# Kernel optimization log

Measured on AMD Instinct MI355X. Metric: run time of the kernel, lower is better.

Reference implementation:

```python
import jax, jax.numpy as jnp
import numpy as np

SELF_DIM = 64
OBST_DIM = 32
NUM_LANDMARKS = 8
HID = 128
IN_DIM = SELF_DIM + OBST_DIM  # 96


def setup_inputs() -> dict:
    key = jax.random.key(0)
    ks = jax.random.split(key, 16)
    B = 1024
    obs = jax.random.normal(ks[0], (B, 1, SELF_DIM + 40 + NUM_LANDMARKS * OBST_DIM), dtype=jnp.float32)

    def w(k, shape, fan_in):
        return (jax.random.normal(k, shape, dtype=jnp.float32) / np.sqrt(fan_in)).astype(jnp.float32)

    return {
        "obs": obs,
        "all_neighbor_obs_size": 40,
        "batch_size": B,
        # Hypernet2: Linear(96->128), tanh, Linear(128->96*128), tanh
        "hw1": w(ks[1], (IN_DIM, HID), IN_DIM), "hb1": jnp.zeros((HID,), jnp.float32),
        "hw2": w(ks[2], (HID, IN_DIM * HID), HID), "hb2": jnp.zeros((IN_DIM * HID,), jnp.float32),
        # neighbor_value_mlp: two Linear(128->128) with tanh
        "vw1": w(ks[3], (HID, HID), HID), "vb1": jnp.zeros((HID,), jnp.float32),
        "vw2": w(ks[4], (HID, HID), HID), "vb2": jnp.zeros((HID,), jnp.float32),
        # attention_mlp: Linear(256->128) tanh, Linear(128->128) tanh, Linear(128->1)
        "aw1": w(ks[5], (2 * HID, HID), 2 * HID), "ab1": jnp.zeros((HID,), jnp.float32),
        "aw2": w(ks[6], (HID, HID), HID), "ab2": jnp.zeros((HID,), jnp.float32),
        "aw3": w(ks[7], (HID, 1), HID), "ab3": jnp.zeros((1,), jnp.float32),
    }


def reference(obs, all_neighbor_obs_size, batch_size,
              hw1, hb1, hw2, hb2, vw1, vb1, vw2, vb2,
              aw1, ab1, aw2, ab2, aw3, ab3):
    B = batch_size
    A = obs.shape[1]  # agents per row (1)
    L = NUM_LANDMARKS

    # slice obstacle block and flatten to per-obstacle rows  [B*A*L, OBST_DIM]
    obs_obstacles = obs[:, :, SELF_DIM + all_neighbor_obs_size:].reshape(-1, OBST_DIM)
    # repeat self-obs along dim 1 (torch .repeat(1, L, 1)) -> [B*A*L, SELF_DIM]
    self_rep = jnp.tile(obs[:, :, :SELF_DIM], (1, L, 1)).reshape(-1, SELF_DIM)
    mlp_input = jnp.concatenate([self_rep, obs_obstacles], axis=1)  # [N, 96]
    N = mlp_input.shape[0]

    # Hypernet2 -> per-instance weight [N, 96, HID]
    h = jnp.tanh(mlp_input @ hw1 + hb1)
    w_flat = jnp.tanh(h @ hw2 + hb2)
    obstacle_w = w_flat.reshape(N, IN_DIM, HID)

    # per-instance matvec + tanh  [N, HID]
    emb = jnp.tanh(jnp.einsum('ni,nio->no', mlp_input, obstacle_w))

    # neighbor value MLP
    vals = jnp.tanh(jnp.tanh(emb @ vw1 + vb1) @ vw2 + vb2)

    # mean pooling over landmarks per batch
    emb_mean = emb.reshape(B, -1, HID).mean(axis=1)  # [B, HID]
    # torch mean.repeat(L, 1): tile whole batch block L times (faithful ordering)
    mean_rep = jnp.tile(emb_mean, (L, 1))  # [B*L, HID]

    att_in = jnp.concatenate([emb, mean_rep], axis=1)  # [N, 2*HID]
    a = jnp.tanh(att_in @ aw1 + ab1)
    a = jnp.tanh(a @ aw2 + ab2)
    logits = (a @ aw3 + ab3).reshape(B, -1)  # [B, L]
    att = jax.nn.softmax(logits, axis=1).reshape(-1, 1)  # [N, 1]

    final = (att * vals).reshape(B, -1, HID).sum(axis=1)  # [B, HID]
    return final.reshape(-1, A, HID)
```

## Files before the change

kernel.cpp:

```cpp
#include <hip/hip_runtime.h>

typedef _Float16 f16x8 __attribute__((ext_vector_type(8)));
typedef float f32x4 __attribute__((ext_vector_type(4)));
typedef const __attribute__((address_space(1))) void* as1_cvp;
typedef __attribute__((address_space(3))) void* as3_vp;

#define LOG2E2 2.88539008177793f

__device__ __forceinline__ float tanh_fast(float x){
  float e = __builtin_amdgcn_exp2f(x * LOG2E2);
  return 1.f - 2.f * __builtin_amdgcn_rcpf(1.f + e);
}
__device__ __forceinline__ unsigned short f2h(float f){
  return __builtin_bit_cast(unsigned short, (_Float16)f);
}
__device__ __forceinline__ float h2f(unsigned short u){
  return (float)__builtin_bit_cast(_Float16, u);
}
__device__ __forceinline__ f32x4 mfma16(f16x8 a, f16x8 b, f32x4 c){
  return __builtin_amdgcn_mfma_f32_16x16x32_f16(a, b, c, 0, 0, 0);
}
__device__ __forceinline__ f16x8 ldsA(const unsigned short* buf, int rb, int s, int lane){
  return *(const f16x8*)(buf + (rb*16 + (lane&15))*128 + s*32 + ((lane>>4)<<3));
}

__global__ __launch_bounds__(256) void prep_kernel(
    const float* __restrict__ obs, const float* __restrict__ hw1,
    const float* __restrict__ hb1, const float* __restrict__ hw2,
    const float* __restrict__ vw1, const float* __restrict__ vw2,
    const float* __restrict__ aw1, const float* __restrict__ aw2,
    unsigned short* __restrict__ wt2, unsigned short* __restrict__ vw1t,
    unsigned short* __restrict__ vw2t, unsigned short* __restrict__ aw1t,
    unsigned short* __restrict__ aw2t, unsigned short* __restrict__ h16,
    float* __restrict__ xT){
  int b = blockIdx.x, t = threadIdx.x;
  if (b < 768){
    __shared__ float xp[64][33];
    int i = b >> 3, chalf = (b&7) >> 2, kq = b & 3;
    int c0 = i*128 + chalf*64, r0 = kq*32;
    int tx = t & 63, j0 = t >> 6;
    #pragma unroll
    for (int j = j0; j < 32; j += 4)
      xp[tx][j] = hw2[(size_t)(r0+j)*12288 + c0 + tx];
    __syncthreads();
    int c = t & 63, kgl = t >> 6;
    unsigned short us[8];
    #pragma unroll
    for (int q=0;q<8;++q) us[q] = f2h(xp[c][kgl*8 + q]);
    size_t dst = (size_t)(i*2 + chalf)*8192 + (size_t)(kq*4 + kgl)*512 + c*8;
    *(uint4*)(wt2 + dst) = *(uint4*)us;
  } else if (b < 848){
    __shared__ float tile[32][33];
    const float* in; unsigned short* out; int R, bx, by;
    if (b < 784)      { int q=b-768; in=vw1; out=vw1t; R=128; bx=q&3; by=q>>2; }
    else if (b < 800) { int q=b-784; in=vw2; out=vw2t; R=128; bx=q&3; by=q>>2; }
    else if (b < 832) { int q=b-800; in=aw1; out=aw1t; R=256; bx=q&3; by=q>>2; }
    else              { int q=b-832; in=aw2; out=aw2t; R=128; bx=q&3; by=q>>2; }
    int c0=bx*32, r0=by*32, tx=t&31, ty=t>>5;
    #pragma unroll
    for (int j=ty; j<32; j+=8) tile[j][tx] = in[(size_t)(r0+j)*128 + c0 + tx];
    __syncthreads();
    #pragma unroll
    for (int j=ty; j<32; j+=8) out[(size_t)(c0+j)*R + r0 + tx] = f2h(tile[tx][j]);
  } else {
    __shared__ float w_s[96*128];
    __shared__ float x_s[32*97];
    __shared__ float b_s[128];
    int n0 = (b-848)*32;
    for (int idx=t; idx<96*128; idx+=256) w_s[idx] = hw1[idx];
    if (t < 128) b_s[t] = hb1[t];
    for (int idx=t; idx<32*96; idx+=256){
      int r = idx/96, i = idx - r*96;
      int n = n0 + r; int bb = n>>3, l = n&7;
      x_s[r*97+i] = (i<64) ? obs[bb*360 + i] : obs[bb*360 + 104 + (l<<5) + (i-64)];
    }
    __syncthreads();
    for (int e=t; e<96*32; e+=256){
      int i = e>>5, r = e&31;
      xT[(size_t)i*8192 + n0 + r] = x_s[r*97 + i];
    }
    for (int e=t; e<32*128; e+=256){
      int r = e>>7, o = e&127;
      float acc = b_s[o];
      const float* xr = &x_s[r*97];
      #pragma unroll 4
      for (int i=0;i<96;++i) acc = fmaf(xr[i], w_s[i*128+o], acc);
      h16[(size_t)(n0+r)*128 + o] = f2h(tanh_fast(acc));
    }
  }
}

__device__ __forceinline__ void stage_tile(const unsigned short* gsrc,
                                           unsigned short* lbuf, int t){
  const unsigned short* g = gsrc + t*8;
  unsigned short* l = lbuf + t*8;
  #pragma unroll
  for (int p=0;p<4;++p)
    __builtin_amdgcn_global_load_lds((as1_cvp)(g + p*2048), (as3_vp)(l + p*2048), 16, 0, 0);
}

__global__ __launch_bounds__(256) __attribute__((amdgpu_waves_per_eu(3,4)))
void k2_hyper(const float* __restrict__ xT, const unsigned short* __restrict__ h16,
              const unsigned short* __restrict__ wt2, const float* __restrict__ hb2,
              float* __restrict__ accg){
  __shared__ unsigned short bts[2][8192];
  __shared__ float x_s[12*128];
  __shared__ float bias_s[12*64];
  int t = threadIdx.x, lane = t & 63, rg = t >> 6;
  int bid = blockIdx.x;
  int rt = bid >> 4, chalf = (bid >> 3) & 1, iseg = bid & 7;
  int R0 = rt*128, C0 = chalf*64, ibase = iseg*12;
  int cl   = lane & 15;
  int g    = lane >> 4;
  int kof  = g << 3;
  int rloc = g << 2;

  for (int idx=t; idx<12*128; idx+=256){
    int il = idx>>7, r = idx&127;
    x_s[idx] = xT[(size_t)(ibase+il)*8192 + R0 + r];
  }
  for (int idx=t; idx<12*64; idx+=256){
    int il = idx>>6, c = idx&63;
    bias_s[idx] = hb2[(ibase+il)*128 + C0 + c];
  }

  f16x8 af[2][4];
  #pragma unroll
  for (int rb=0; rb<2; ++rb)
    #pragma unroll
    for (int s=0; s<4; ++s)
      af[rb][s] = *(const f16x8*)(h16 + (size_t)(R0 + rg*32 + rb*16 + cl)*128 + s*32 + kof);

  stage_tile(wt2 + (size_t)(ibase*2 + chalf)*8192, bts[0], t);

  float facc[2][4][4];
  #pragma unroll
  for (int rb=0;rb<2;++rb)
    #pragma unroll
    for (int ch=0;ch<4;++ch)
      #pragma unroll
      for (int reg=0;reg<4;++reg) facc[rb][ch][reg] = 0.f;

  const f32x4 zero4 = {0.f,0.f,0.f,0.f};

  for (int it=0; it<12; ++it){
    asm volatile("s_waitcnt vmcnt(0)" ::: "memory");
    __builtin_amdgcn_s_barrier();
    __builtin_amdgcn_sched_barrier(0);
    const unsigned short* lb = bts[it&1];
    if (it < 11) stage_tile(wt2 + (size_t)((ibase+it+1)*2 + chalf)*8192, bts[(it+1)&1], t);

    f32x4 xa = *(const f32x4*)(x_s + it*128 + rg*32 + rloc);
    f32x4 xb = *(const f32x4*)(x_s + it*128 + rg*32 + 16 + rloc);
    #pragma unroll
    for (int ch=0; ch<4; ++ch){
      int c64 = ch*16 + cl;
      const unsigned short* bp = lb + c64*8 + g*512;
      f16x8 b0 = *(const f16x8*)(bp);
      f16x8 b1 = *(const f16x8*)(bp + 2048);
      f16x8 b2 = *(const f16x8*)(bp + 4096);
      f16x8 b3 = *(const f16x8*)(bp + 6144);
      float bi2 = bias_s[it*64 + c64] * LOG2E2;
      f32x4 a0 = zero4, a1 = zero4;
      a0 = mfma16(af[0][0], b0, a0); a1 = mfma16(af[1][0], b0, a1);
      a0 = mfma16(af[0][1], b1, a0); a1 = mfma16(af[1][1], b1, a1);
      a0 = mfma16(af[0][2], b2, a0); a1 = mfma16(af[1][2], b2, a1);
      a0 = mfma16(af[0][3], b3, a0); a1 = mfma16(af[1][3], b3, a1);
      #pragma unroll
      for (int reg=0;reg<4;++reg){
        float e0 = __builtin_amdgcn_exp2f(fmaf(a0[reg], LOG2E2, bi2));
        float e1 = __builtin_amdgcn_exp2f(fmaf(a1[reg], LOG2E2, bi2));
        float t0 = 1.f - 2.f*__builtin_amdgcn_rcpf(1.f + e0);
        float t1 = 1.f - 2.f*__builtin_amdgcn_rcpf(1.f + e1);
        facc[0][ch][reg] = fmaf(xa[reg], t0, facc[0][ch][reg]);
        facc[1][ch][reg] = fmaf(xb[reg], t1, facc[1][ch][reg]);
      }
    }
  }

  #pragma unroll
  for (int rb=0; rb<2; ++rb)
    #pragma unroll
    for (int ch=0; ch<4; ++ch)
      #pragma unroll
      for (int reg=0; reg<4; ++reg)
        atomicAdd(&accg[(size_t)(R0 + rg*32 + rb*16 + rloc + reg)*128 + C0 + ch*16 + cl],
                  facc[rb][ch][reg]);
}

__global__ __launch_bounds__(256) void k3_mean(const float* __restrict__ accg,
    unsigned short* __restrict__ mean16){
  int t = threadIdx.x, B0 = blockIdx.x*4;
  for (int task=t; task<512; task+=256){
    int bl = task>>7, o = task&127;
    float m = 0.f;
    #pragma unroll
    for (int l=0;l<8;++l)
      m += tanh_fast(accg[(size_t)((B0 + bl)*8 + l)*128 + o]);
    mean16[(size_t)(B0 + bl)*128 + o] = f2h(m * 0.125f);
  }
}

template<int KS>
__device__ __forceinline__ void stage(const unsigned short* inA, const unsigned short* inB,
    const unsigned short* wt, const float* bias, unsigned short* outb, int w, int lane){
  #pragma unroll
  for (int obl=0; obl<2; ++obl){
    int col = ((w*2+obl)<<4) + (lane&15);
    f32x4 a0 = {0.f,0.f,0.f,0.f}, a1v = {0.f,0.f,0.f,0.f};
    #pragma unroll
    for (int s=0;s<KS;++s){
      f16x8 bfr = *(const f16x8*)(wt + (size_t)col*(KS*32) + s*32 + ((lane>>4)<<3));
      f16x8 aa0, aa1;
      if (KS==8 && s>=4){ aa0 = ldsA(inB,0,s-4,lane); aa1 = ldsA(inB,1,s-4,lane); }
      else              { aa0 = ldsA(inA,0,s,lane);   aa1 = ldsA(inA,1,s,lane);   }
      a0  = mfma16(aa0, bfr, a0);
      a1v = mfma16(aa1, bfr, a1v);
    }
    float bb = bias[col];
    #pragma unroll
    for (int reg=0;reg<4;++reg){
      int r0 = ((lane>>4)<<2) + reg;
      outb[r0*128 + col]      = f2h(tanh_fast(a0[reg] + bb));
      outb[(16+r0)*128 + col] = f2h(tanh_fast(a1v[reg] + bb));
    }
  }
}

__global__ __launch_bounds__(256) void k4_mlp(
    const float* __restrict__ accg, const unsigned short* __restrict__ mean16,
    const unsigned short* __restrict__ vw1t, const unsigned short* __restrict__ vw2t,
    const unsigned short* __restrict__ aw1t, const unsigned short* __restrict__ aw2t,
    const float* __restrict__ vb1, const float* __restrict__ vb2,
    const float* __restrict__ ab1, const float* __restrict__ ab2,
    const float* __restrict__ aw3, const float* __restrict__ ab3,
    float* __restrict__ outp){
  __shared__ unsigned short bufE[32*128];
  __shared__ unsigned short bufM[32*128];
  __shared__ unsigned short bufA[32*128];
  __shared__ float fin[4*128];
  __shared__ float lp[32*8];
  __shared__ float att_s[32];
  int t = threadIdx.x, lane = t&63, w = t>>6;
  int R0 = blockIdx.x*32;

  for (int idx=t; idx<4096; idx+=256)
    bufE[idx] = f2h(tanh_fast(accg[(size_t)R0*128 + idx]));
  for (int idx=t; idx<512; idx+=256){
    int r = idx>>4, c8 = (idx&15)<<3;
    int n = R0 + r;
    *(uint4*)(bufM + r*128 + c8) = *(const uint4*)(mean16 + (size_t)(n & 1023)*128 + c8);
  }
  for (int idx=t; idx<512; idx+=256) fin[idx] = 0.f;
  __syncthreads();

  stage<8>(bufE, bufM, aw1t, ab1, bufA, w, lane);
  __syncthreads();
  stage<4>(bufA, nullptr, aw2t, ab2, bufM, w, lane);
  __syncthreads();
  {
    int r = t>>3, seg = t&7;
    float p = 0.f;
    const unsigned short* row = bufM + r*128 + seg*16;
    const float* w3 = aw3 + seg*16;
    #pragma unroll
    for (int k=0;k<16;++k) p += h2f(row[k]) * w3[k];
    lp[r*8+seg] = p;
  }
  __syncthreads();
  if (t < 4){
    float lg[8]; float mx = -1e30f;
    for (int l=0;l<8;++l){
      float s = ab3[0];
      #pragma unroll
      for (int sg=0;sg<8;++sg) s += lp[(t*8+l)*8+sg];
      lg[l] = s; mx = fmaxf(mx, s);
    }
    float sum = 0.f;
    for (int l=0;l<8;++l){ lg[l] = __builtin_amdgcn_exp2f((lg[l]-mx)*1.44269504089f); sum += lg[l]; }
    float inv = __builtin_amdgcn_rcpf(sum);
    for (int l=0;l<8;++l) att_s[t*8+l] = lg[l]*inv;
  }
  __syncthreads();
  stage<4>(bufE, nullptr, vw1t, vb1, bufA, w, lane);
  __syncthreads();
  {
    #pragma unroll
    for (int obl=0; obl<2; ++obl){
      int col = ((w*2+obl)<<4) + (lane&15);
      f32x4 a0 = {0.f,0.f,0.f,0.f}, a1v = {0.f,0.f,0.f,0.f};
      #pragma unroll
      for (int s=0;s<4;++s){
        f16x8 bfr = *(const f16x8*)(vw2t + (size_t)col*128 + s*32 + ((lane>>4)<<3));
        a0  = mfma16(ldsA(bufA,0,s,lane), bfr, a0);
        a1v = mfma16(ldsA(bufA,1,s,lane), bfr, a1v);
      }
      float bb = vb2[col];
      #pragma unroll
      for (int reg=0;reg<4;++reg){
        int r0 = ((lane>>4)<<2) + reg;
        float v0 = tanh_fast(a0[reg]+bb);
        float v1 = tanh_fast(a1v[reg]+bb);
        atomicAdd(&fin[((r0)>>3)*128 + col],    att_s[r0]    * v0);
        atomicAdd(&fin[((16+r0)>>3)*128 + col], att_s[16+r0] * v1);
      }
    }
  }
  __syncthreads();
  for (int idx=t; idx<512; idx+=256){
    int b_loc = idx>>7, o = idx&127;
    outp[(size_t)(R0/8 + b_loc)*128 + o] = fin[idx];
  }
}

extern "C" void kernel_launch(void* const* d_in, const int* in_sizes, int n_in,
                              void* d_out, int out_size, void* d_ws, size_t ws_size,
                              hipStream_t stream){
  const float* obs = (const float*)d_in[0];
  const float* hw1 = (const float*)d_in[3];
  const float* hb1 = (const float*)d_in[4];
  const float* hw2 = (const float*)d_in[5];
  const float* hb2 = (const float*)d_in[6];
  const float* vw1 = (const float*)d_in[7];
  const float* vb1 = (const float*)d_in[8];
  const float* vw2 = (const float*)d_in[9];
  const float* vb2 = (const float*)d_in[10];
  const float* aw1 = (const float*)d_in[11];
  const float* ab1 = (const float*)d_in[12];
  const float* aw2 = (const float*)d_in[13];
  const float* ab2 = (const float*)d_in[14];
  const float* aw3 = (const float*)d_in[15];
  const float* ab3 = (const float*)d_in[16];

  char* ws = (char*)d_ws;
  unsigned short* wt2    = (unsigned short*)(ws);
  unsigned short* mean16 = (unsigned short*)(ws);
  unsigned short* h16    = (unsigned short*)(ws + 3145728);
  float*          accg   = (float*)        (ws + 5242880);
  float*          xT     = (float*)        (ws + 9437184);
  unsigned short* vw1t   = (unsigned short*)(ws + 12582912);
  unsigned short* vw2t   = (unsigned short*)(ws + 12615680);
  unsigned short* aw1t   = (unsigned short*)(ws + 12648448);
  unsigned short* aw2t   = (unsigned short*)(ws + 12713984);
  float* outp = (float*)d_out;

  hipMemsetAsync(accg, 0, 8192*128*sizeof(float), stream);
  prep_kernel<<<1104, 256, 0, stream>>>(obs, hw1, hb1, hw2, vw1, vw2, aw1, aw2,
                                        wt2, vw1t, vw2t, aw1t, aw2t, h16, xT);
  k2_hyper<<<1024, 256, 0, stream>>>(xT, h16, wt2, hb2, accg);
  k3_mean<<<256, 256, 0, stream>>>(accg, mean16);
  k4_mlp<<<256, 256, 0, stream>>>(accg, mean16, vw1t, vw2t, aw1t, aw2t,
                                  vb1, vb2, ab1, ab2, aw3, ab3, outp);
}
```

Measured before the change: 118.6 us.

## Fuse accumulator zeroing into prep and mean pooling into hyper kernel

Removes the hipMemsetAsync and the separate k3_mean launch. The accumulator is now zeroed inside prep_kernel, and the last k2_hyper block for each row tile (picked with an atomic counter) applies tanh, writes fp16 embeddings and computes the landmark means. k4 then reads the fp16 embeddings directly. The k2 barrier is moved to the end of each loop iteration, the bias is stored pre-scaled in fp16 in a shared-memory union, and the first tile's staging is issued earlier. The risks are a serialized tail in the last-arriving blocks, the extra fence and atomic reads, and a small precision loss from the fp16 bias.

```diff
diff --git a/kernel.cpp b/kernel.cpp
--- a/kernel.cpp
+++ b/kernel.cpp
@@ -32,8 +32,15 @@
     unsigned short* __restrict__ wt2, unsigned short* __restrict__ vw1t,
     unsigned short* __restrict__ vw2t, unsigned short* __restrict__ aw1t,
     unsigned short* __restrict__ aw2t, unsigned short* __restrict__ h16,
-    float* __restrict__ xT){
+    float* __restrict__ xT, float* __restrict__ accg, int* __restrict__ cnt){
   int b = blockIdx.x, t = threadIdx.x;
+  if (b < 256){
+    f32x4 z = {0.f,0.f,0.f,0.f};
+    #pragma unroll
+    for (int i=t; i<1024; i+=256) ((f32x4*)accg)[(size_t)b*1024 + i] = z;
+  }
+  if (b == 848 && t < 64) cnt[t] = 0;
+
   if (b < 768){
     __shared__ float xp[64][33];
     int i = b >> 3, chalf = (b&7) >> 2, kq = b & 3;
@@ -102,10 +109,16 @@
 __global__ __launch_bounds__(256) __attribute__((amdgpu_waves_per_eu(3,4)))
 void k2_hyper(const float* __restrict__ xT, const unsigned short* __restrict__ h16,
               const unsigned short* __restrict__ wt2, const float* __restrict__ hb2,
-              float* __restrict__ accg){
-  __shared__ unsigned short bts[2][8192];
-  __shared__ float x_s[12*128];
-  __shared__ float bias_s[12*64];
+              float* __restrict__ accg, int* __restrict__ cnt,
+              unsigned short* __restrict__ emb16, unsigned short* __restrict__ mean16){
+  __shared__ char smem[40448];
+  unsigned short* bts0 = (unsigned short*)smem;
+  unsigned short* bts1 = (unsigned short*)(smem + 16384);
+  float* x_s           = (float*)(smem + 32768);
+  unsigned short* bias_s = (unsigned short*)(smem + 38912);
+  int* lastflag        = (int*)(smem + 32768);
+  unsigned short* es   = (unsigned short*)smem;
+
   int t = threadIdx.x, lane = t & 63, rg = t >> 6;
   int bid = blockIdx.x;
   int rt = bid >> 4, chalf = (bid >> 3) & 1, iseg = bid & 7;
@@ -115,13 +128,15 @@
   int kof  = g << 3;
   int rloc = g << 2;
 
+  stage_tile(wt2 + (size_t)(ibase*2 + chalf)*8192, bts0, t);
+
   for (int idx=t; idx<12*128; idx+=256){
     int il = idx>>7, r = idx&127;
     x_s[idx] = xT[(size_t)(ibase+il)*8192 + R0 + r];
   }
   for (int idx=t; idx<12*64; idx+=256){
     int il = idx>>6, c = idx&63;
-    bias_s[idx] = hb2[(ibase+il)*128 + C0 + c];
+    bias_s[idx] = f2h(hb2[(ibase+il)*128 + C0 + c] * LOG2E2);
   }
 
   f16x8 af[2][4];
@@ -131,8 +146,6 @@
     for (int s=0; s<4; ++s)
       af[rb][s] = *(const f16x8*)(h16 + (size_t)(R0 + rg*32 + rb*16 + cl)*128 + s*32 + kof);
 
-  stage_tile(wt2 + (size_t)(ibase*2 + chalf)*8192, bts[0], t);
-
   float facc[2][4][4];
   #pragma unroll
   for (int rb=0;rb<2;++rb)
@@ -141,14 +154,16 @@
       #pragma unroll
       for (int reg=0;reg<4;++reg) facc[rb][ch][reg] = 0.f;
 
+  asm volatile("s_waitcnt vmcnt(0) lgkmcnt(0)" ::: "memory");
+  __builtin_amdgcn_s_barrier();
+  __builtin_amdgcn_sched_barrier(0);
+
   const f32x4 zero4 = {0.f,0.f,0.f,0.f};
 
   for (int it=0; it<12; ++it){
-    asm volatile("s_waitcnt vmcnt(0)" ::: "memory");
-    __builtin_amdgcn_s_barrier();
-    __builtin_amdgcn_sched_barrier(0);
-    const unsigned short* lb = bts[it&1];
-    if (it < 11) stage_tile(wt2 + (size_t)((ibase+it+1)*2 + chalf)*8192, bts[(it+1)&1], t);
+    const unsigned short* lb = (it & 1) ? bts1 : bts0;
+    if (it < 11)
+      stage_tile(wt2 + (size_t)((ibase+it+1)*2 + chalf)*8192, (it&1)?bts0:bts1, t);
 
     f32x4 xa = *(const f32x4*)(x_s + it*128 + rg*32 + rloc);
     f32x4 xb = *(const f32x4*)(x_s + it*128 + rg*32 + 16 + rloc);
@@ -160,7 +175,7 @@
       f16x8 b1 = *(const f16x8*)(bp + 2048);
       f16x8 b2 = *(const f16x8*)(bp + 4096);
       f16x8 b3 = *(const f16x8*)(bp + 6144);
-      float bi2 = bias_s[it*64 + c64] * LOG2E2;
+      float bi2 = h2f(bias_s[it*64 + c64]);
       f32x4 a0 = zero4, a1 = zero4;
       a0 = mfma16(af[0][0], b0, a0); a1 = mfma16(af[1][0], b0, a1);
       a0 = mfma16(af[0][1], b1, a0); a1 = mfma16(af[1][1], b1, a1);
@@ -176,6 +191,9 @@
         facc[1][ch][reg] = fmaf(xb[reg], t1, facc[1][ch][reg]);
       }
     }
+    asm volatile("s_waitcnt vmcnt(0)" ::: "memory");
+    __builtin_amdgcn_s_barrier();
+    __builtin_amdgcn_sched_barrier(0);
   }
 
   #pragma unroll
@@ -186,18 +204,28 @@
       for (int reg=0; reg<4; ++reg)
         atomicAdd(&accg[(size_t)(R0 + rg*32 + rb*16 + rloc + reg)*128 + C0 + ch*16 + cl],
                   facc[rb][ch][reg]);
-}
-
-__global__ __launch_bounds__(256) void k3_mean(const float* __restrict__ accg,
-    unsigned short* __restrict__ mean16){
-  int t = threadIdx.x, B0 = blockIdx.x*4;
-  for (int task=t; task<512; task+=256){
-    int bl = task>>7, o = task&127;
+
+  __threadfence();
+  __syncthreads();
+  if (t == 0) *lastflag = (atomicAdd(&cnt[rt], 1) == 15) ? 1 : 0;
+  __syncthreads();
+  if (!*lastflag) return;
+
+  for (int idx=t; idx<128*128; idx+=256){
+    int row = idx>>7, col = idx&127;
+    float v = atomicAdd(&accg[(size_t)(R0+row)*128 + col], 0.f);
+    float e = tanh_fast(v);
+    unsigned short h = f2h(e);
+    es[idx] = h;
+    emb16[(size_t)(R0+row)*128 + col] = h;
+  }
+  __syncthreads();
+  for (int task=t; task<16*128; task+=256){
+    int bl = task>>7, col = task&127;
     float m = 0.f;
     #pragma unroll
-    for (int l=0;l<8;++l)
-      m += tanh_fast(accg[(size_t)((B0 + bl)*8 + l)*128 + o]);
-    mean16[(size_t)(B0 + bl)*128 + o] = f2h(m * 0.125f);
+    for (int l=0;l<8;++l) m += h2f(es[(bl*8+l)*128 + col]);
+    mean16[(size_t)(rt*16 + bl)*128 + col] = f2h(m * 0.125f);
   }
 }
 
@@ -228,7 +256,7 @@
 }
 
 __global__ __launch_bounds__(256) void k4_mlp(
-    const float* __restrict__ accg, const unsigned short* __restrict__ mean16,
+    const unsigned short* __restrict__ emb16, const unsigned short* __restrict__ mean16,
     const unsigned short* __restrict__ vw1t, const unsigned short* __restrict__ vw2t,
     const unsigned short* __restrict__ aw1t, const unsigned short* __restrict__ aw2t,
     const float* __restrict__ vb1, const float* __restrict__ vb2,
@@ -244,11 +272,10 @@
   int t = threadIdx.x, lane = t&63, w = t>>6;
   int R0 = blockIdx.x*32;
 
-  for (int idx=t; idx<4096; idx+=256)
-    bufE[idx] = f2h(tanh_fast(accg[(size_t)R0*128 + idx]));
   for (int idx=t; idx<512; idx+=256){
     int r = idx>>4, c8 = (idx&15)<<3;
     int n = R0 + r;
+    *(uint4*)(bufE + r*128 + c8) = *(const uint4*)(emb16  + (size_t)n*128 + c8);
     *(uint4*)(bufM + r*128 + c8) = *(const uint4*)(mean16 + (size_t)(n & 1023)*128 + c8);
   }
   for (int idx=t; idx<512; idx+=256) fin[idx] = 0.f;
@@ -334,21 +361,21 @@
 
   char* ws = (char*)d_ws;
   unsigned short* wt2    = (unsigned short*)(ws);
-  unsigned short* mean16 = (unsigned short*)(ws);
   unsigned short* h16    = (unsigned short*)(ws + 3145728);
   float*          accg   = (float*)        (ws + 5242880);
   float*          xT     = (float*)        (ws + 9437184);
-  unsigned short* vw1t   = (unsigned short*)(ws + 12582912);
-  unsigned short* vw2t   = (unsigned short*)(ws + 12615680);
-  unsigned short* aw1t   = (unsigned short*)(ws + 12648448);
-  unsigned short* aw2t   = (unsigned short*)(ws + 12713984);
+  unsigned short* emb16  = (unsigned short*)(ws + 12582912);
+  unsigned short* mean16 = (unsigned short*)(ws + 14680064);
+  unsigned short* vw1t   = (unsigned short*)(ws + 14942208);
+  unsigned short* vw2t   = (unsigned short*)(ws + 14974976);
+  unsigned short* aw1t   = (unsigned short*)(ws + 15007744);
+  unsigned short* aw2t   = (unsigned short*)(ws + 15073280);
+  int*            cnt    = (int*)           (ws + 15106048);
   float* outp = (float*)d_out;
 
-  hipMemsetAsync(accg, 0, 8192*128*sizeof(float), stream);
   prep_kernel<<<1104, 256, 0, stream>>>(obs, hw1, hb1, hw2, vw1, vw2, aw1, aw2,
-                                        wt2, vw1t, vw2t, aw1t, aw2t, h16, xT);
-  k2_hyper<<<1024, 256, 0, stream>>>(xT, h16, wt2, hb2, accg);
-  k3_mean<<<256, 256, 0, stream>>>(accg, mean16);
-  k4_mlp<<<256, 256, 0, stream>>>(accg, mean16, vw1t, vw2t, aw1t, aw2t,
+                                        wt2, vw1t, vw2t, aw1t, aw2t, h16, xT, accg, cnt);
+  k2_hyper<<<1024, 256, 0, stream>>>(xT, h16, wt2, hb2, accg, cnt, emb16, mean16);
+  k4_mlp<<<256, 256, 0, stream>>>(emb16, mean16, vw1t, vw2t, aw1t, aw2t,
                                   vb1, vb2, ab1, ab2, aw3, ab3, outp);
 }
```

Result: slower. 193.2 us (+62.9%).
